# Kernel optimization log

Measured on AMD Instinct MI355X. Metric: run time of the kernel, lower is better.

The kernel has to match this reference:

```python
import jax, jax.numpy as jnp
import numpy as np
from jax import lax

B, S, D = 256, 2048, 64

def setup_inputs() -> dict:
    key = jax.random.key(0)
    k1, k2, k3 = jax.random.split(key, 3)
    y_pred = jax.random.normal(k1, (B, S, D), dtype=jnp.float32)
    y_true = jax.random.randint(k2, (B, S), 0, D, dtype=jnp.int64)
    mask = jnp.ones((B, S), dtype=jnp.float32)
    trans = jax.random.uniform(k3, (D, D), dtype=jnp.float32, minval=-0.1, maxval=0.1)
    return {"y_pred": y_pred, "y_true": y_true, "mask": mask, "trans": trans}

def reference(y_pred, y_true, mask, trans):
    # mask -> [B,S,1] float, applied to emissions and one-hot targets
    m = mask.astype(y_pred.dtype)[:, :, None]
    yp = y_pred * m                                      # [B,S,D]
    y1h = jax.nn.one_hot(y_true, trans.shape[0], dtype=y_pred.dtype) * m  # [B,S,D]

    # target score: emission + transition along gold path
    point_score = jnp.einsum('bni,bni->b', yp, y1h)
    trans_score = jnp.einsum('bni,ij,bnj->b', y1h[:, :-1], trans, y1h[:, 1:])
    target = point_score + trans_score                   # [B]

    # forward algorithm (log partition) as a scan over seq_len
    state0 = yp[:, 0]                                    # [B,D]
    emis = jnp.swapaxes(yp[:, 1:], 0, 1)                 # [S-1,B,D]
    msk = jnp.swapaxes(m[:, 1:], 0, 1)                   # [S-1,B,1]

    def step(state, xs):
        e, cm = xs                                       # e:[B,D], cm:[B,1]
        # logsumexp over previous tag: state[B,prev,1] + trans[prev,next]
        scores = state[:, :, None] + trans[None, :, :]   # [B,D,D]
        out = jax.scipy.special.logsumexp(scores, axis=1) + e
        new_state = cm * out + (1.0 - cm) * state
        return new_state, None

    final, _ = lax.scan(step, state0, (emis, msk))
    log_norm = jax.scipy.special.logsumexp(final, axis=1)  # [B]
    return log_norm - target
```

## Files before the change

kernel.cpp:

```cpp
#include <hip/hip_runtime.h>


#define B_   256
#define S_   2048
#define D_   64
#define CHK  128
#define CL   16
#define WUP  8

typedef float  f32x4 __attribute__((ext_vector_type(4)));
typedef short  v4s   __attribute__((ext_vector_type(4)));

#if __has_builtin(__builtin_amdgcn_mfma_f32_16x16x16bf16_1k)
static __device__ __forceinline__ f32x4 mfma16(v4s a, v4s b, f32x4 cc) {
    return __builtin_amdgcn_mfma_f32_16x16x16bf16_1k(a, b, cc, 0, 0, 0);
}
#else
static __device__ __forceinline__ f32x4 mfma16(v4s a, v4s b, f32x4 cc) {
    f32x4 d;
    asm("v_mfma_f32_16x16x16_bf16 %0, %1, %2, %3"
        : "=&v"(d) : "v"(a), "v"(b), "v"(cc));
    return d;
}
#endif

static __device__ __forceinline__ unsigned bf16_rne(float x) {
    unsigned u = __float_as_uint(x);
    u += 0x7fffu + ((u >> 16) & 1u);
    return u >> 16;
}
static __device__ __forceinline__ float bf2f(short h) {
    return __uint_as_float(((unsigned)(unsigned short)h) << 16);
}
static __device__ __forceinline__ v4s pack4(float a, float b, float c2, float d) {
    union { uint2 u; v4s s; } uu;
    uu.u.x = bf16_rne(a) | (bf16_rne(b) << 16);
    uu.u.y = bf16_rne(c2) | (bf16_rne(d) << 16);
    return uu.s;
}

__global__ __launch_bounds__(256) void target_kernel(
    const float* __restrict__ y_pred, const int* __restrict__ y_true,
    const float* __restrict__ mask, const float* __restrict__ trans,
    float* __restrict__ target)
{
    int b = blockIdx.x;
    int tid = threadIdx.x;
    const int*   yt = y_true + (size_t)b * S_;
    const float* mk = mask   + (size_t)b * S_;
    const float* yp = y_pred + (size_t)b * S_ * D_;

    float acc = 0.f;
    for (int n = tid; n < S_; n += 256) {
        int   tn = yt[n];
        float mn = mk[n];
        acc += mn * mn * yp[(size_t)n * D_ + tn];
        if (n + 1 < S_) {
            int   tn1 = yt[n + 1];
            float mn1 = mk[n + 1];
            acc += mn * mn1 * trans[tn * D_ + tn1];
        }
    }
    #pragma unroll
    for (int m = 32; m >= 1; m >>= 1) acc += __shfl_xor(acc, m, 64);
    __shared__ float sred[4];
    int wid = tid >> 6;
    if ((tid & 63) == 0) sred[wid] = acc;
    __syncthreads();
    if (tid == 0) target[b] = sred[0] + sred[1] + sred[2] + sred[3];
}

__global__ __launch_bounds__(64, 2) void mfma_chunk_scan(
    const float* __restrict__ y_pred, const float* __restrict__ mask,
    const float* __restrict__ trans, float* __restrict__ partials)
{
    const int u  = blockIdx.x;
    const int bg = u & 15;
    const int c  = u >> 4;
    const int l  = threadIdx.x;
    const int g  = l >> 4, cb = l & 15;
    const int b0 = bg * 16;
    const float* yprowc = y_pred + (size_t)(b0 + cb) * S_ * D_;
    const float* mrowc  = mask   + (size_t)(b0 + cb) * S_;

    v4s Av[4][4];
    #pragma unroll
    for (int m = 0; m < 4; ++m)
        #pragma unroll
        for (int kt = 0; kt < 4; ++kt) {
            float a0 = __expf(trans[(16*kt + 4*g + 0) * D_ + 16*m + cb]);
            float a1 = __expf(trans[(16*kt + 4*g + 1) * D_ + 16*m + cb]);
            float a2 = __expf(trans[(16*kt + 4*g + 2) * D_ + 16*m + cb]);
            float a3 = __expf(trans[(16*kt + 4*g + 3) * D_ + 16*m + cb]);
            Av[m][kt] = pack4(a0, a1, a2, a3);
        }

    v4s Bv[4];
    if (c == 0) {
        float m0 = mrowc[0];
        #pragma unroll
        for (int kt = 0; kt < 4; ++kt) {
            float p0 = __expf(yprowc[16*kt + 4*g + 0] * m0);
            float p1 = __expf(yprowc[16*kt + 4*g + 1] * m0);
            float p2 = __expf(yprowc[16*kt + 4*g + 2] * m0);
            float p3 = __expf(yprowc[16*kt + 4*g + 3] * m0);
            Bv[kt] = pack4(p0, p1, p2, p3);
        }
    } else {
        const short one = (short)0x3f80;
        v4s vone = {one, one, one, one};
        #pragma unroll
        for (int kt = 0; kt < 4; ++kt) Bv[kt] = vone;
    }

    int K = 0;
    const f32x4 zf = {0.f, 0.f, 0.f, 0.f};

    auto mag = [&]() -> double {
        float s = 0.f;
        #pragma unroll
        for (int m = 0; m < 4; ++m)
            s += (bf2f(Bv[m][0]) + bf2f(Bv[m][1])) +
                 (bf2f(Bv[m][2]) + bf2f(Bv[m][3]));
        s += __shfl_xor(s, 16, 64);
        s += __shfl_xor(s, 32, 64);
        return (double)K * 0.6931471805599453 + (double)__logf(s);
    };

    const int t0    = (c == 0) ? 1 : CL * c - (WUP - 1);
    const int t_end = (CL * (c + 1) > S_ - 1) ? (S_ - 1) : CL * (c + 1);
    const int rec_t = CL * c;
    double m_start = 0.0;

    auto step = [&](int t, float4 e0, float4 e1, float4 e2, float4 e3, float cm) {
        f32x4 acc[4];
        #pragma unroll
        for (int m = 0; m < 4; ++m) acc[m] = mfma16(Av[m][0], Bv[0], zf);
        #pragma unroll
        for (int kt = 1; kt < 4; ++kt)
            #pragma unroll
            for (int m = 0; m < 4; ++m)
                acc[m] = mfma16(Av[m][kt], Bv[kt], acc[m]);

        float4 ee[4] = {e0, e1, e2, e3};
        f32x4 pr[4];
        if (__builtin_expect(__all(cm == 1.0f), 1)) {
            #pragma unroll
            for (int m = 0; m < 4; ++m) {
                pr[m][0] = acc[m][0] * __expf(ee[m].x);
                pr[m][1] = acc[m][1] * __expf(ee[m].y);
                pr[m][2] = acc[m][2] * __expf(ee[m].z);
                pr[m][3] = acc[m][3] * __expf(ee[m].w);
            }
        } else {
            #pragma unroll
            for (int m = 0; m < 4; ++m) {
                float er[4] = {ee[m].x, ee[m].y, ee[m].z, ee[m].w};
                #pragma unroll
                for (int e = 0; e < 4; ++e) {
                    float sum  = acc[m][e];
                    float pold = bf2f(Bv[m][e]);
                    float pn;
                    if (cm == 1.0f) {
                        pn = sum * __expf(er[e]);
                    } else {
                        float outn = __logf(sum) + er[e] * cm;
                        float oldl = __logf(pold);
                        pn = __expf(cm * outn + (1.f - cm) * oldl);
                    }
                    pr[m][e] = pn;
                }
            }
        }

        if ((t & 3) == 0) {
            unsigned rep = __builtin_amdgcn_readfirstlane(__float_as_uint(pr[0][0]));
            int k = (int)((rep >> 23) & 0xffu) - 127;
            k = k < -110 ? -110 : (k > 110 ? 110 : k);
            float sc = __uint_as_float((unsigned)(127 - k) << 23);
            #pragma unroll
            for (int m = 0; m < 4; ++m) {
                pr[m][0] *= sc; pr[m][1] *= sc; pr[m][2] *= sc; pr[m][3] *= sc;
            }
            K += k;
        }

        #pragma unroll
        for (int m = 0; m < 4; ++m)
            Bv[m] = pack4(pr[m][0], pr[m][1], pr[m][2], pr[m][3]);

        if (c > 0 && t == rec_t) m_start = mag();
    };

    float4 EA0, EA1, EA2, EA3, EB0, EB1, EB2, EB3;
    float  cmA, cmB;
    auto loadA = [&](int t) {
        int tt = t > t_end ? t_end : t;
        const float* base = yprowc + (size_t)tt * D_ + 4 * g;
        EA0 = *(const float4*)(base +  0); EA1 = *(const float4*)(base + 16);
        EA2 = *(const float4*)(base + 32); EA3 = *(const float4*)(base + 48);
        cmA = mrowc[tt];
    };
    auto loadB = [&](int t) {
        int tt = t > t_end ? t_end : t;
        const float* base = yprowc + (size_t)tt * D_ + 4 * g;
        EB0 = *(const float4*)(base +  0); EB1 = *(const float4*)(base + 16);
        EB2 = *(const float4*)(base + 32); EB3 = *(const float4*)(base + 48);
        cmB = mrowc[tt];
    };

    loadA(t0); loadB(t0 + 1);
    for (int t = t0; t <= t_end; t += 2) {
        {
            float4 e0 = EA0, e1 = EA1, e2 = EA2, e3 = EA3; float cm = cmA;
            loadA(t + 2);
            step(t, e0, e1, e2, e3, cm);
        }
        if (t + 1 <= t_end) {
            float4 e0 = EB0, e1 = EB1, e2 = EB2, e3 = EB3; float cm = cmB;
            loadB(t + 3);
            step(t + 1, e0, e1, e2, e3, cm);
        }
    }

    double delta = mag() - m_start;
    if (l < 16) partials[(size_t)(b0 + l) * CHK + c] = (float)delta;
}

__global__ __launch_bounds__(256) void combine_kernel(
    const float* __restrict__ partials, const float* __restrict__ target,
    float* __restrict__ out)
{
    int b = blockIdx.x * 256 + threadIdx.x;
    if (b >= B_) return;
    double acc = 0.0;
    for (int c = 0; c < CHK; ++c) acc += (double)partials[(size_t)b * CHK + c];
    out[b] = (float)acc - target[b];
}

extern "C" void kernel_launch(void* const* d_in, const int* in_sizes, int n_in,
                              void* d_out, int out_size, void* d_ws, size_t ws_size,
                              hipStream_t stream)
{
    const float* y_pred = (const float*)d_in[0];
    const int*   y_true = (const int*)d_in[1];
    const float* mask   = (const float*)d_in[2];
    const float* trans  = (const float*)d_in[3];
    float* outp     = (float*)d_out;
    float* target   = (float*)d_ws;
    float* partials = (float*)((char*)d_ws + 4096);

    hipLaunchKernelGGL(target_kernel, dim3(B_), dim3(256), 0, stream,
                       y_pred, y_true, mask, trans, target);
    hipLaunchKernelGGL(mfma_chunk_scan, dim3(16 * CHK), dim3(64), 0, stream,
                       y_pred, mask, trans, partials);
    hipLaunchKernelGGL(combine_kernel, dim3(1), dim3(256), 0, stream,
                       partials, target, outp);
}
```

Measured before the change: 64.82 us.

## Fuse target kernel into chunk scan, halve chunk count, deepen emission prefetch

Merges the target-score kernel into the chunked scan launch as extra 64-thread blocks, removing one kernel launch. Chunk count drops from 128 to 64 with 32-step chunks, so the fixed warm-up overhead per chunk is paid fewer times, but each block's serial chain gets longer. Emission loads are now prefetched in groups of four timesteps with double buffering, which raises register pressure (launch bounds changed to 1 block min).

Result: slower. 69.06 us (+6.5%).

```diff
diff --git a/kernel.cpp b/kernel.cpp
--- a/kernel.cpp
+++ b/kernel.cpp
@@ -4,9 +4,10 @@
 #define B_   256
 #define S_   2048
 #define D_   64
-#define CHK  128
-#define CL   16
+#define CHK  64
+#define CL   32
 #define WUP  8
+#define SCAN_BLKS (16 * CHK)
 
 typedef float  f32x4 __attribute__((ext_vector_type(4)));
 typedef short  v4s   __attribute__((ext_vector_type(4)));
@@ -39,45 +40,38 @@
     return uu.s;
 }
 
-__global__ __launch_bounds__(256) void target_kernel(
+__global__ __launch_bounds__(64, 1) void fused_scan_target(
     const float* __restrict__ y_pred, const int* __restrict__ y_true,
     const float* __restrict__ mask, const float* __restrict__ trans,
-    float* __restrict__ target)
+    float* __restrict__ partials, float* __restrict__ target)
 {
-    int b = blockIdx.x;
-    int tid = threadIdx.x;
-    const int*   yt = y_true + (size_t)b * S_;
-    const float* mk = mask   + (size_t)b * S_;
-    const float* yp = y_pred + (size_t)b * S_ * D_;
-
-    float acc = 0.f;
-    for (int n = tid; n < S_; n += 256) {
-        int   tn = yt[n];
-        float mn = mk[n];
-        acc += mn * mn * yp[(size_t)n * D_ + tn];
-        if (n + 1 < S_) {
-            int   tn1 = yt[n + 1];
-            float mn1 = mk[n + 1];
-            acc += mn * mn1 * trans[tn * D_ + tn1];
-        }
+    const int l = threadIdx.x;
+
+    if (blockIdx.x >= SCAN_BLKS) {
+        int b = blockIdx.x - SCAN_BLKS;
+        const int*   yt = y_true + (size_t)b * S_;
+        const float* mk = mask   + (size_t)b * S_;
+        const float* yp = y_pred + (size_t)b * S_ * D_;
+        float acc = 0.f;
+        for (int n = l; n < S_; n += 64) {
+            int   tn = yt[n];
+            float mn = mk[n];
+            acc += mn * mn * yp[(size_t)n * D_ + tn];
+            if (n + 1 < S_) {
+                int   tn1 = yt[n + 1];
+                float mn1 = mk[n + 1];
+                acc += mn * mn1 * trans[tn * D_ + tn1];
+            }
+        }
+        #pragma unroll
+        for (int m = 32; m >= 1; m >>= 1) acc += __shfl_xor(acc, m, 64);
+        if (l == 0) target[b] = acc;
+        return;
     }
-    #pragma unroll
-    for (int m = 32; m >= 1; m >>= 1) acc += __shfl_xor(acc, m, 64);
-    __shared__ float sred[4];
-    int wid = tid >> 6;
-    if ((tid & 63) == 0) sred[wid] = acc;
-    __syncthreads();
-    if (tid == 0) target[b] = sred[0] + sred[1] + sred[2] + sred[3];
-}
-
-__global__ __launch_bounds__(64, 2) void mfma_chunk_scan(
-    const float* __restrict__ y_pred, const float* __restrict__ mask,
-    const float* __restrict__ trans, float* __restrict__ partials)
-{
+
     const int u  = blockIdx.x;
     const int bg = u & 15;
     const int c  = u >> 4;
-    const int l  = threadIdx.x;
     const int g  = l >> 4, cb = l & 15;
     const int b0 = bg * 16;
     const float* yprowc = y_pred + (size_t)(b0 + cb) * S_ * D_;
@@ -132,7 +126,7 @@
     const int rec_t = CL * c;
     double m_start = 0.0;
 
-    auto step = [&](int t, float4 e0, float4 e1, float4 e2, float4 e3, float cm) {
+    auto step = [&](int t, const float4 (&ee)[4], float cm) {
         f32x4 acc[4];
         #pragma unroll
         for (int m = 0; m < 4; ++m) acc[m] = mfma16(Av[m][0], Bv[0], zf);
@@ -142,7 +136,6 @@
             for (int m = 0; m < 4; ++m)
                 acc[m] = mfma16(Av[m][kt], Bv[kt], acc[m]);
 
-        float4 ee[4] = {e0, e1, e2, e3};
         f32x4 pr[4];
         if (__builtin_expect(__all(cm == 1.0f), 1)) {
             #pragma unroll
@@ -188,38 +181,54 @@
         #pragma unroll
         for (int m = 0; m < 4; ++m)
             Bv[m] = pack4(pr[m][0], pr[m][1], pr[m][2], pr[m][3]);
-
-        if (c > 0 && t == rec_t) m_start = mag();
-    };
-
-    float4 EA0, EA1, EA2, EA3, EB0, EB1, EB2, EB3;
-    float  cmA, cmB;
-    auto loadA = [&](int t) {
-        int tt = t > t_end ? t_end : t;
-        const float* base = yprowc + (size_t)tt * D_ + 4 * g;
-        EA0 = *(const float4*)(base +  0); EA1 = *(const float4*)(base + 16);
-        EA2 = *(const float4*)(base + 32); EA3 = *(const float4*)(base + 48);
-        cmA = mrowc[tt];
-    };
-    auto loadB = [&](int t) {
-        int tt = t > t_end ? t_end : t;
-        const float* base = yprowc + (size_t)tt * D_ + 4 * g;
-        EB0 = *(const float4*)(base +  0); EB1 = *(const float4*)(base + 16);
-        EB2 = *(const float4*)(base + 32); EB3 = *(const float4*)(base + 48);
-        cmB = mrowc[tt];
-    };
-
-    loadA(t0); loadB(t0 + 1);
-    for (int t = t0; t <= t_end; t += 2) {
-        {
-            float4 e0 = EA0, e1 = EA1, e2 = EA2, e3 = EA3; float cm = cmA;
-            loadA(t + 2);
-            step(t, e0, e1, e2, e3, cm);
-        }
-        if (t + 1 <= t_end) {
-            float4 e0 = EB0, e1 = EB1, e2 = EB2, e3 = EB3; float cm = cmB;
-            loadB(t + 3);
-            step(t + 1, e0, e1, e2, e3, cm);
+    };
+
+    float4 EA[4][4], EB[4][4];
+    float  cmA[4], cmB[4];
+    auto loadA = [&](int tg) {
+        #pragma unroll
+        for (int s = 0; s < 4; ++s) {
+            int tt = tg + s; if (tt > t_end) tt = t_end;
+            const float* base = yprowc + (size_t)tt * D_ + 4 * g;
+            EA[s][0] = *(const float4*)(base +  0);
+            EA[s][1] = *(const float4*)(base + 16);
+            EA[s][2] = *(const float4*)(base + 32);
+            EA[s][3] = *(const float4*)(base + 48);
+            cmA[s] = mrowc[tt];
+        }
+    };
+    auto loadB = [&](int tg) {
+        #pragma unroll
+        for (int s = 0; s < 4; ++s) {
+            int tt = tg + s; if (tt > t_end) tt = t_end;
+            const float* base = yprowc + (size_t)tt * D_ + 4 * g;
+            EB[s][0] = *(const float4*)(base +  0);
+            EB[s][1] = *(const float4*)(base + 16);
+            EB[s][2] = *(const float4*)(base + 32);
+            EB[s][3] = *(const float4*)(base + 48);
+            cmB[s] = mrowc[tt];
+        }
+    };
+
+    loadA(t0);
+    for (int tg = t0; tg <= t_end; tg += 8) {
+        loadB(tg + 4);
+        #pragma unroll
+        for (int s = 0; s < 4; ++s) {
+            int t = tg + s;
+            if (t <= t_end) {
+                step(t, EA[s], cmA[s]);
+                if (c > 0 && t == rec_t) m_start = mag();
+            }
+        }
+        loadA(tg + 8);
+        #pragma unroll
+        for (int s = 0; s < 4; ++s) {
+            int t = tg + 4 + s;
+            if (t <= t_end) {
+                step(t, EB[s], cmB[s]);
+                if (c > 0 && t == rec_t) m_start = mag();
+            }
         }
     }
 
@@ -250,10 +259,8 @@
     float* target   = (float*)d_ws;
     float* partials = (float*)((char*)d_ws + 4096);
 
-    hipLaunchKernelGGL(target_kernel, dim3(B_), dim3(256), 0, stream,
-                       y_pred, y_true, mask, trans, target);
-    hipLaunchKernelGGL(mfma_chunk_scan, dim3(16 * CHK), dim3(64), 0, stream,
-                       y_pred, mask, trans, partials);
+    hipLaunchKernelGGL(fused_scan_target, dim3(SCAN_BLKS + B_), dim3(64), 0,
+                       stream, y_pred, y_true, mask, trans, partials, target);
     hipLaunchKernelGGL(combine_kernel, dim3(1), dim3(256), 0, stream,
                        partials, target, outp);
 }
```
